# Optimization experiments

Measured on AMD Instinct MI355X. Metric: run time of the kernel, lower is better.

The kernel has to match this reference:

```python
import jax, jax.numpy as jnp
import numpy as np

B, S, F, D, H, L = 32, 512, 40, 512, 8, 4
T = S + 1
DK, DV = D // 2, D          # expand_k=0.5, expand_v=1.0 (fla GLA defaults)
HK, HV = DK // H, DV // H
GLR = 16                    # gate low-rank dim
GLN = 16.0                  # gate logit normalizer
MLP = 4 * D


def sin_pos(t, d, n=10000.0):
    pos = jnp.arange(t, dtype=jnp.float32)[:, None]
    den = jnp.power(n, 2.0 * jnp.arange(d // 2, dtype=jnp.float32) / d)
    e = jnp.zeros((t, d), jnp.float32)
    e = e.at[:, 0::2].set(jnp.sin(pos / den))
    e = e.at[:, 1::2].set(jnp.cos(pos / den))
    return e


def layernorm(x, w, b, eps=1e-5):
    m = x.mean(-1, keepdims=True)
    v = ((x - m) ** 2).mean(-1, keepdims=True)
    return (x - m) * jax.lax.rsqrt(v + eps) * w + b


def bin_norm(x, l1, b1, l2, b2, y1, y2):
    # x: (b, f, s). BiN: temporal z-norm with per-feature affine (X2) +
    # feature z-norm with per-time affine (X1); unbiased std, small std -> 1.
    st = jnp.sqrt(x.var(axis=2, ddof=1, keepdims=True))
    st = jnp.where(st < 1e-4, 1.0, st)
    Z2 = (x - x.mean(axis=2, keepdims=True)) / st
    X2 = l2[None, :, None] * Z2 + b2[None, :, None]
    sf = jnp.sqrt(x.var(axis=1, ddof=1, keepdims=True))
    sf = jnp.where(sf < 1e-4, 1.0, sf)
    Z1 = (x - x.mean(axis=1, keepdims=True)) / sf
    X1 = l1[None, None, :] * Z1 + b1[None, None, :]
    return y1 * X1 + y2 * X2


def gla_attn(x, qw, kw, vw, gw, gkw1, gkw2, gkb2, gnw, ow):
    # Gated linear attention, recurrent form: S_t = exp(gk_t) * S_{t-1} + k_t v_t^T
    b, t, _ = x.shape
    q = (x @ qw).reshape(b, t, H, HK) * (HK ** -0.5)
    k = (x @ kw).reshape(b, t, H, HK)
    v = (x @ vw).reshape(b, t, H, HV)
    g = (x @ gw).reshape(b, t, H, HV)
    gk = (jax.nn.log_sigmoid((x @ gkw1) @ gkw2 + gkb2) / GLN).reshape(b, t, H, HK)

    def step(Sc, inp):
        qt, kt, vt, gt = inp                       # (b,H,HK),(b,H,HK),(b,H,HV),(b,H,HK)
        Sc = Sc * jnp.exp(gt)[..., None] + kt[..., None] * vt[..., None, :]
        return Sc, jnp.einsum('bhk,bhkv->bhv', qt, Sc)

    init = jnp.zeros((b, H, HK, HV), x.dtype)
    to_t = lambda a: jnp.swapaxes(a, 0, 1)        # (t, b, H, dim)
    _, o = jax.lax.scan(step, init, (to_t(q), to_t(k), to_t(v), to_t(gk)))
    o = jnp.swapaxes(o, 0, 1)                     # (b, t, H, HV)
    o = o * jax.lax.rsqrt((o * o).mean(-1, keepdims=True) + 1e-5) * gnw  # head RMSNorm
    o = o * g * jax.nn.sigmoid(g)                 # swish output gate
    return o.reshape(b, t, DV) @ ow


def setup_inputs():
    key = jax.random.key(0)
    ks = iter(jax.random.split(key, 64))
    r = lambda shape, s=0.02: jax.random.normal(next(ks), shape, jnp.float32) * s
    return dict(
        x=jax.random.normal(next(ks), (B, S, F), jnp.float32),
        bin_l1=r((S,), 0.1), bin_b1=jnp.zeros((S,), jnp.float32),
        bin_l2=r((F,), 0.1), bin_b2=jnp.zeros((F,), jnp.float32),
        bin_y1=jnp.float32(0.5), bin_y2=jnp.float32(0.5),
        emb_w=r((F, D)), emb_b=jnp.zeros((D,), jnp.float32),
        cls_token=jnp.zeros((D,), jnp.float32),
        ln1_w=jnp.ones((L, D), jnp.float32), ln1_b=jnp.zeros((L, D), jnp.float32),
        q_w=r((L, D, DK)), k_w=r((L, D, DK)), v_w=r((L, D, DV)), g_w=r((L, D, DV)),
        gk_w1=r((L, D, GLR)), gk_w2=r((L, GLR, DK)), gk_b2=jnp.zeros((L, DK), jnp.float32),
        gnorm_w=jnp.ones((L, HV), jnp.float32),
        o_w=r((L, DV, D)),
        ln2_w=jnp.ones((L, D), jnp.float32), ln2_b=jnp.zeros((L, D), jnp.float32),
        mlp_w1=r((L, D, MLP)), mlp_b1=jnp.zeros((L, MLP), jnp.float32),
        mlp_w2=r((L, MLP, D)), mlp_b2=jnp.zeros((L, D), jnp.float32),
        head_w=r((D, 3)), head_b=jnp.zeros((3,), jnp.float32),
    )


def reference(x, bin_l1, bin_b1, bin_l2, bin_b2, bin_y1, bin_y2, emb_w, emb_b,
              cls_token, ln1_w, ln1_b, q_w, k_w, v_w, g_w, gk_w1, gk_w2, gk_b2,
              gnorm_w, o_w, ln2_w, ln2_b, mlp_w1, mlp_b1, mlp_w2, mlp_b2,
              head_w, head_b):
    h = bin_norm(jnp.swapaxes(x, 1, 2), bin_l1, bin_b1, bin_l2, bin_b2, bin_y1, bin_y2)
    h = jnp.swapaxes(h, 1, 2) @ emb_w + emb_b                    # (b, s, D)
    cls = jnp.broadcast_to(cls_token, (h.shape[0], 1, D))
    h = jnp.concatenate([h, cls], axis=1) + sin_pos(T, D)[None]  # (b, s+1, D)
    for i in range(L):
        a = gla_attn(layernorm(h, ln1_w[i], ln1_b[i]), q_w[i], k_w[i], v_w[i],
                     g_w[i], gk_w1[i], gk_w2[i], gk_b2[i], gnorm_w[i], o_w[i])
        h = h + a
        m = layernorm(h, ln2_w[i], ln2_b[i])
        m = jax.nn.gelu(m @ mlp_w1[i] + mlp_b1[i], approximate=False)
        h = h + m @ mlp_w2[i] + mlp_b2[i]
    return h[:, -1] @ head_w + head_b                            # (b, 3)
```

## Files before the change

### kernel.cpp

```cpp
#include <hip/hip_runtime.h>
#include <hip/hip_bf16.h>
#include <math.h>

#define Bsz   32
#define Ssz   512
#define Fsz   40
#define Dsz   512
#define Hh    8
#define Lnum  4
#define Tsz   513
#define DKsz  256
#define DVsz  512
#define HKsz  32
#define HVsz  64
#define Msz   (Bsz*Tsz)
#define Mpad  16512
#define MLPsz 2048
#define NCH   8
#define CSZ   65
#define QKVG  1536

typedef __attribute__((ext_vector_type(4))) float f32x4;
typedef __attribute__((ext_vector_type(8))) short bf16x8;

__device__ __forceinline__ float bf2f(short s) {
  unsigned int u = ((unsigned int)(unsigned short)s) << 16;
  return __builtin_bit_cast(float, u);
}
__device__ __forceinline__ short f2bf(float f) {
  __hip_bfloat16 b = __float2bfloat16(f);
  return __builtin_bit_cast(short, b);
}

__device__ __forceinline__ float wave_sum(float v) {
#pragma unroll
  for (int off = 32; off > 0; off >>= 1) v += __shfl_xor(v, off, 64);
  return v;
}

__global__ void pos_kernel(float* __restrict__ pos) {
  int idx = blockIdx.x * 256 + threadIdx.x;
  if (idx >= Tsz * Dsz) return;
  int t = idx / Dsz, d = idx % Dsz;
  float e = (float)(2 * (d >> 1)) / (float)Dsz;
  float den = powf(10000.f, e);
  float a = (float)t / den;
  pos[idx] = (d & 1) ? cosf(a) : sinf(a);
}

__global__ void tstat_kernel(const float* __restrict__ x,
                             float* __restrict__ mt, float* __restrict__ rst) {
  int bf = blockIdx.x;
  int b = bf / Fsz, f = bf % Fsz;
  int lane = threadIdx.x;
  const float* xp = x + (size_t)b * Ssz * Fsz + f;
  float s = 0.f, sq = 0.f;
  for (int i = lane; i < Ssz; i += 64) {
    float v = xp[(size_t)i * Fsz];
    s += v; sq += v * v;
  }
  s = wave_sum(s); sq = wave_sum(sq);
  if (lane == 0) {
    float m = s / (float)Ssz;
    float var = (sq - (float)Ssz * m * m) / (float)(Ssz - 1);
    float st = sqrtf(fmaxf(var, 0.f));
    if (st < 1e-4f) st = 1.f;
    mt[bf] = m;
    rst[bf] = 1.f / st;
  }
}

__global__ __launch_bounds__(64) void binorm_kernel(
    const float* __restrict__ x, const float* __restrict__ l1,
    const float* __restrict__ b1, const float* __restrict__ l2,
    const float* __restrict__ b2, const float* __restrict__ y1p,
    const float* __restrict__ y2p, const float* __restrict__ mt,
    const float* __restrict__ rst, float* __restrict__ xbT) {
  int row = blockIdx.x;
  int lane = threadIdx.x;
  int b = row / Tsz, t = row % Tsz;
  bool valid = (row < Msz) && (t < Ssz);
  if (!valid) {
    if (lane < Fsz) xbT[(size_t)lane * Mpad + row] = 0.f;
    return;
  }
  float xv = 0.f;
  const float* xp = x + ((size_t)b * Ssz + t) * Fsz;
  if (lane < Fsz) xv = xp[lane];
  float s  = wave_sum(lane < Fsz ? xv : 0.f);
  float sq = wave_sum(lane < Fsz ? xv * xv : 0.f);
  float m = s / (float)Fsz;
  float var = (sq - (float)Fsz * m * m) / (float)(Fsz - 1);
  float sf = sqrtf(fmaxf(var, 0.f));
  if (sf < 1e-4f) sf = 1.f;
  if (lane < Fsz) {
    float y1 = y1p[0], y2 = y2p[0];
    float z1 = (xv - m) / sf;
    float X1 = l1[t] * z1 + b1[t];
    int bf = b * Fsz + lane;
    float z2 = (xv - mt[bf]) * rst[bf];
    float X2 = l2[lane] * z2 + b2[lane];
    xbT[(size_t)lane * Mpad + row] = y1 * X1 + y2 * X2;
  }
}

__global__ __launch_bounds__(256, 4) void embgemm_kernel(
    const float* __restrict__ xbT, const float* __restrict__ emb_w,
    const float* __restrict__ emb_b, const float* __restrict__ cls,
    const float* __restrict__ pos, float* __restrict__ h) {
  __shared__ float as[Fsz][64];
  __shared__ float bs[Fsz][64];
  int tid = threadIdx.x, tx = tid & 15, ty = tid >> 4;
  int r0 = blockIdx.x * 64, c0 = blockIdx.y * 64;
  for (int idx = tid; idx < Fsz * 64; idx += 256) {
    int f = idx >> 6, r = idx & 63;
    as[f][r] = xbT[(size_t)f * Mpad + r0 + r];
    bs[f][r] = emb_w[f * Dsz + c0 + r];
  }
  __syncthreads();
  float acc[4][4] = {};
#pragma unroll 5
  for (int f = 0; f < Fsz; ++f) {
    float4 a = *(const float4*)&as[f][ty * 4];
    float4 bv = *(const float4*)&bs[f][tx * 4];
    float av[4] = {a.x, a.y, a.z, a.w};
    float bw[4] = {bv.x, bv.y, bv.z, bv.w};
#pragma unroll
    for (int i = 0; i < 4; ++i)
#pragma unroll
      for (int j = 0; j < 4; ++j) acc[i][j] += av[i] * bw[j];
  }
#pragma unroll
  for (int i = 0; i < 4; ++i) {
    int gm = r0 + ty * 4 + i;
    int t = gm % Tsz;
    const float* pp = pos + (size_t)t * Dsz;
    bool iscls = (t == Ssz);
    int gn = c0 + tx * 4;
#pragma unroll
    for (int j = 0; j < 4; ++j) {
      float v = iscls ? (cls[gn + j] + pp[gn + j])
                      : (acc[i][j] + emb_b[gn + j] + pp[gn + j]);
      h[(size_t)gm * Dsz + gn + j] = v;
    }
  }
}

__global__ __launch_bounds__(64) void ln_kernel(
    const float* __restrict__ in, const float* __restrict__ w,
    const float* __restrict__ b, short* __restrict__ out) {
  int row = blockIdx.x, lane = threadIdx.x;
  const float* p = in + (size_t)row * Dsz;
  float4 v0 = *(const float4*)(p + lane * 8);
  float4 v1 = *(const float4*)(p + lane * 8 + 4);
  float s  = v0.x + v0.y + v0.z + v0.w + v1.x + v1.y + v1.z + v1.w;
  float sq = v0.x*v0.x + v0.y*v0.y + v0.z*v0.z + v0.w*v0.w
           + v1.x*v1.x + v1.y*v1.y + v1.z*v1.z + v1.w*v1.w;
  s = wave_sum(s); sq = wave_sum(sq);
  float m = s * (1.f / Dsz);
  float var = sq * (1.f / Dsz) - m * m;
  float r = rsqrtf(var + 1e-5f);
  float4 w0 = *(const float4*)(w + lane * 8);
  float4 w1 = *(const float4*)(w + lane * 8 + 4);
  float4 b0 = *(const float4*)(b + lane * 8);
  float4 b1v = *(const float4*)(b + lane * 8 + 4);
  bf16x8 pk;
  pk[0] = f2bf((v0.x - m) * r * w0.x + b0.x);
  pk[1] = f2bf((v0.y - m) * r * w0.y + b0.y);
  pk[2] = f2bf((v0.z - m) * r * w0.z + b0.z);
  pk[3] = f2bf((v0.w - m) * r * w0.w + b0.w);
  pk[4] = f2bf((v1.x - m) * r * w1.x + b1v.x);
  pk[5] = f2bf((v1.y - m) * r * w1.y + b1v.y);
  pk[6] = f2bf((v1.z - m) * r * w1.z + b1v.z);
  pk[7] = f2bf((v1.w - m) * r * w1.w + b1v.w);
  *(bf16x8*)(out + (size_t)row * Dsz + lane * 8) = pk;
}

__global__ __launch_bounds__(256) void wt_kernel(const float* __restrict__ W,
    short* __restrict__ Wt, int K, int N) {
  __shared__ float t[32][33];
  int k0 = blockIdx.x * 32, n0 = blockIdx.y * 32;
  int tx = threadIdx.x & 31, ty = threadIdx.x >> 5;
#pragma unroll
  for (int r = 0; r < 32; r += 8)
    t[ty + r][tx] = W[(size_t)(k0 + ty + r) * N + n0 + tx];
  __syncthreads();
#pragma unroll
  for (int r = 0; r < 32; r += 8)
    Wt[(size_t)(n0 + ty + r) * K + k0 + tx] = f2bf(t[tx][ty + r]);
}

__global__ __launch_bounds__(256) void wt4_kernel(const float* __restrict__ qw,
    const float* __restrict__ kw, const float* __restrict__ vw,
    const float* __restrict__ gw, short* __restrict__ Wt) {
  __shared__ float t[32][33];
  int k0 = blockIdx.x * 32, n0g = blockIdx.y * 32;
  const float* W; int n0, ld;
  if (n0g < 256)       { W = qw; n0 = n0g;        ld = DKsz; }
  else if (n0g < 512)  { W = kw; n0 = n0g - 256;  ld = DKsz; }
  else if (n0g < 1024) { W = vw; n0 = n0g - 512;  ld = DVsz; }
  else                 { W = gw; n0 = n0g - 1024; ld = DVsz; }
  int tx = threadIdx.x & 31, ty = threadIdx.x >> 5;
#pragma unroll
  for (int r = 0; r < 32; r += 8)
    t[ty + r][tx] = W[(size_t)(k0 + ty + r) * ld + n0 + tx];
  __syncthreads();
#pragma unroll
  for (int r = 0; r < 32; r += 8)
    Wt[(size_t)(n0g + ty + r) * Dsz + k0 + tx] = f2bf(t[tx][ty + r]);
}

template<int ACT, int OBF>
__global__ __launch_bounds__(256) void mgemm_kernel(
    const short* __restrict__ A, const short* __restrict__ Bt,
    void* __restrict__ Cv, const float* __restrict__ bias,
    const float* __restrict__ resid, int N, int K) {
  __shared__ short As[128 * 64];
  __shared__ short Bs[128 * 64];
  int tid = threadIdx.x;
  int lane = tid & 63, wid = tid >> 6;
  int wr = wid >> 1, wc = wid & 1;
  int m0 = blockIdx.x * 128, n0 = blockIdx.y * 128;
  f32x4 acc[4][4];
#pragma unroll
  for (int i = 0; i < 4; ++i)
#pragma unroll
    for (int j = 0; j < 4; ++j) acc[i][j] = (f32x4){0.f, 0.f, 0.f, 0.f};

  int kq = lane >> 4;
  int rsel = lane & 15;

  for (int kt = 0; kt < K; kt += 64) {
#pragma unroll
    for (int i = 0; i < 4; ++i) {
      int li = i * 256 + tid;
      int row = li >> 3;
      int gsrc = (li & 7) ^ (row & 7);
      const short* ga = A + (size_t)(m0 + row) * K + kt + gsrc * 8;
      const short* gb = Bt + (size_t)(n0 + row) * K + kt + gsrc * 8;
      int base = (i * 256 + wid * 64) * 8;
      __builtin_amdgcn_global_load_lds(
          (const __attribute__((address_space(1))) unsigned int*)ga,
          (__attribute__((address_space(3))) unsigned int*)&As[base], 16, 0, 0);
      __builtin_amdgcn_global_load_lds(
          (const __attribute__((address_space(1))) unsigned int*)gb,
          (__attribute__((address_space(3))) unsigned int*)&Bs[base], 16, 0, 0);
    }
    __syncthreads();
#pragma unroll
    for (int s = 0; s < 2; ++s) {
      bf16x8 af[4], bfr[4];
#pragma unroll
      for (int i = 0; i < 4; ++i) {
        int row = wr * 64 + i * 16 + rsel;
        int slot = (s * 4 + kq) ^ (row & 7);
        af[i] = *(const bf16x8*)&As[row * 64 + slot * 8];
        int col = wc * 64 + i * 16 + rsel;
        int slotB = (s * 4 + kq) ^ (col & 7);
        bfr[i] = *(const bf16x8*)&Bs[col * 64 + slotB * 8];
      }
#pragma unroll
      for (int i = 0; i < 4; ++i)
#pragma unroll
        for (int j = 0; j < 4; ++j)
          acc[i][j] = __builtin_amdgcn_mfma_f32_16x16x32_bf16(af[i], bfr[j], acc[i][j], 0, 0, 0);
    }
    __syncthreads();
  }

#pragma unroll
  for (int i = 0; i < 4; ++i) {
    int rbase = m0 + wr * 64 + i * 16 + (lane >> 4) * 4;
#pragma unroll
    for (int j = 0; j < 4; ++j) {
      int gn = n0 + wc * 64 + j * 16 + (lane & 15);
      float bv = bias ? bias[gn] : 0.f;
#pragma unroll
      for (int r = 0; r < 4; ++r) {
        int gm = rbase + r;
        float v = acc[i][j][r] + bv;
        if (ACT == 1) v = 0.5f * v * (1.f + erff(v * 0.70710678118654752f));
        if (resid) v += resid[(size_t)gm * N + gn];
        if (OBF) ((short*)Cv)[(size_t)gm * N + gn] = f2bf(v);
        else     ((float*)Cv)[(size_t)gm * N + gn] = v;
      }
    }
  }
}

__global__ __launch_bounds__(64) void gk1_kernel(const short* __restrict__ xn,
    const float* __restrict__ w1, float* __restrict__ gk1) {
  int m = blockIdx.x, lane = threadIdx.x;
  __shared__ float xr[512];
  bf16x8 v = *(const bf16x8*)(xn + (size_t)m * Dsz + lane * 8);
#pragma unroll
  for (int e = 0; e < 8; ++e) xr[lane * 8 + e] = bf2f(v[e]);
  __syncthreads();
  int c = lane & 15, q = lane >> 4;
  float acc = 0.f;
#pragma unroll 8
  for (int i = 0; i < 128; ++i) {
    int k = q * 128 + i;
    acc += xr[k] * w1[k * 16 + c];
  }
  acc += __shfl_xor(acc, 16, 64);
  acc += __shfl_xor(acc, 32, 64);
  if (lane < 16) gk1[(size_t)m * 16 + c] = acc;
}

__global__ __launch_bounds__(256) void gk2_kernel(
    const float* __restrict__ gk1, const float* __restrict__ w2,
    const float* __restrict__ b2, float* __restrict__ gke) {
  int m = blockIdx.x, n = threadIdx.x;
  __shared__ float row[16];
  if (n < 16) row[n] = gk1[(size_t)m * 16 + n];
  __syncthreads();
  float acc = b2[n];
#pragma unroll
  for (int kk = 0; kk < 16; ++kk) acc += row[kk] * w2[kk * 256 + n];
  float z = acc;
  float ls = (z >= 0.f) ? -log1pf(expf(-z)) : z - log1pf(expf(z));
  gke[(size_t)m * 256 + n] = expf(ls * 0.0625f);
}

__global__ __launch_bounds__(64) void scanA_kernel(
    const float* __restrict__ qkvg, const float* __restrict__ gke,
    float* __restrict__ Ac, float* __restrict__ Bc) {
  int gid = blockIdx.x;
  int bh = gid >> 3, c = gid & 7;
  int b = bh >> 3, hh = bh & 7;
  int lane = threadIdx.x;
  int t0 = c * CSZ, t1 = min(t0 + CSZ, Tsz);
  const size_t rb = (size_t)b * Tsz;
  float S[32];
#pragma unroll
  for (int i = 0; i < 32; ++i) S[i] = 0.f;
  float ac = 1.f;
  for (int t = t0; t < t1; ++t) {
    const float* base = qkvg + (rb + t) * QKVG;
    const float* krow = base + 256 + hh * HKsz;
    const float* grow = gke + (rb + t) * DKsz + hh * HKsz;
    float vv = base[512 + hh * HVsz + lane];
    float gl = grow[lane & 31];
    float4 kr[8], gr[8];
#pragma unroll
    for (int j = 0; j < 8; ++j) {
      kr[j] = *(const float4*)(krow + j * 4);
      gr[j] = *(const float4*)(grow + j * 4);
    }
#pragma unroll
    for (int j = 0; j < 8; ++j) {
      S[4*j+0] = S[4*j+0] * gr[j].x + kr[j].x * vv;
      S[4*j+1] = S[4*j+1] * gr[j].y + kr[j].y * vv;
      S[4*j+2] = S[4*j+2] * gr[j].z + kr[j].z * vv;
      S[4*j+3] = S[4*j+3] * gr[j].w + kr[j].w * vv;
    }
    ac *= gl;
  }
  float* bp = Bc + ((size_t)gid * 64 + lane) * 32;
#pragma unroll
  for (int j = 0; j < 8; ++j)
    *(float4*)(bp + j * 4) = make_float4(S[4*j+0], S[4*j+1], S[4*j+2], S[4*j+3]);
  if (lane < 32) Ac[(size_t)gid * 32 + lane] = ac;
}

__global__ __launch_bounds__(64) void scanB_kernel(
    const float* __restrict__ Ac, float* __restrict__ Bc) {
  int bh = blockIdx.x;
  int lane = threadIdx.x;
  float cur[32];
#pragma unroll
  for (int i = 0; i < 32; ++i) cur[i] = 0.f;
  __shared__ float sA[32];
  for (int c = 0; c < NCH; ++c) {
    size_t gid = (size_t)bh * NCH + c;
    float* bp = Bc + (gid * 64 + lane) * 32;
    __syncthreads();
    if (lane < 32) sA[lane] = Ac[gid * 32 + lane];
    __syncthreads();
    float4 tb[8];
#pragma unroll
    for (int j = 0; j < 8; ++j) tb[j] = *(const float4*)(bp + j * 4);
#pragma unroll
    for (int j = 0; j < 8; ++j)
      *(float4*)(bp + j * 4) = make_float4(cur[4*j+0], cur[4*j+1], cur[4*j+2], cur[4*j+3]);
#pragma unroll
    for (int j = 0; j < 8; ++j) {
      cur[4*j+0] = sA[4*j+0] * cur[4*j+0] + tb[j].x;
      cur[4*j+1] = sA[4*j+1] * cur[4*j+1] + tb[j].y;
      cur[4*j+2] = sA[4*j+2] * cur[4*j+2] + tb[j].z;
      cur[4*j+3] = sA[4*j+3] * cur[4*j+3] + tb[j].w;
    }
  }
}

__global__ __launch_bounds__(64) void scanC_kernel(
    const float* __restrict__ qkvg, const float* __restrict__ gke,
    const float* __restrict__ gnw, const float* __restrict__ Bc,
    short* __restrict__ att) {
  int gid = blockIdx.x;
  int bh = gid >> 3, c = gid & 7;
  int b = bh >> 3, hh = bh & 7;
  int lane = threadIdx.x;
  int t0 = c * CSZ, t1 = min(t0 + CSZ, Tsz);
  const size_t rb = (size_t)b * Tsz;
  float S[32];
  const float* sp = Bc + ((size_t)gid * 64 + lane) * 32;
#pragma unroll
  for (int j = 0; j < 8; ++j) {
    float4 sv4 = *(const float4*)(sp + j * 4);
    S[4*j+0] = sv4.x; S[4*j+1] = sv4.y; S[4*j+2] = sv4.z; S[4*j+3] = sv4.w;
  }
  float gn = gnw[lane];
  for (int t = t0; t < t1; ++t) {
    const float* base = qkvg + (rb + t) * QKVG;
    const float* qrow = base + hh * HKsz;
    const float* krow = base + 256 + hh * HKsz;
    const float* grow = gke + (rb + t) * DKsz + hh * HKsz;
    float vv = base[512 + hh * HVsz + lane];
    float gv = base[1024 + hh * HVsz + lane];
    float4 kr[8], gr[8], qr[8];
#pragma unroll
    for (int j = 0; j < 8; ++j) {
      qr[j] = *(const float4*)(qrow + j * 4);
      kr[j] = *(const float4*)(krow + j * 4);
      gr[j] = *(const float4*)(grow + j * 4);
    }
    float o = 0.f;
#pragma unroll
    for (int j = 0; j < 8; ++j) {
      S[4*j+0] = S[4*j+0] * gr[j].x + kr[j].x * vv;  o += qr[j].x * S[4*j+0];
      S[4*j+1] = S[4*j+1] * gr[j].y + kr[j].y * vv;  o += qr[j].y * S[4*j+1];
      S[4*j+2] = S[4*j+2] * gr[j].z + kr[j].z * vv;  o += qr[j].z * S[4*j+2];
      S[4*j+3] = S[4*j+3] * gr[j].w + kr[j].w * vv;  o += qr[j].w * S[4*j+3];
    }
    o *= 0.17677669529663689f;
    float ss = wave_sum(o * o);
    float r = rsqrtf(ss * (1.f / 64.f) + 1e-5f);
    float sig = 1.f / (1.f + expf(-gv));
    att[((rb + t) * DVsz) + hh * HVsz + lane] = f2bf(o * r * gn * gv * sig);
  }
}

__global__ __launch_bounds__(64) void head_kernel(
    const float* __restrict__ h, const float* __restrict__ hw,
    const float* __restrict__ hb, float* __restrict__ out) {
  int b = blockIdx.x, lane = threadIdx.x;
  const float* p = h + ((size_t)b * Tsz + Ssz) * Dsz;
  float p0 = 0.f, p1 = 0.f, p2 = 0.f;
#pragma unroll
  for (int j = 0; j < 8; ++j) {
    int d = lane + j * 64;
    float hv = p[d];
    p0 += hv * hw[d * 3 + 0];
    p1 += hv * hw[d * 3 + 1];
    p2 += hv * hw[d * 3 + 2];
  }
  p0 = wave_sum(p0); p1 = wave_sum(p1); p2 = wave_sum(p2);
  if (lane == 0) {
    out[b * 3 + 0] = p0 + hb[0];
    out[b * 3 + 1] = p1 + hb[1];
    out[b * 3 + 2] = p2 + hb[2];
  }
}

extern "C" void kernel_launch(void* const* d_in, const int* in_sizes, int n_in,
                              void* d_out, int out_size, void* d_ws, size_t ws_size,
                              hipStream_t stream) {
  const float* x       = (const float*)d_in[0];
  const float* bin_l1  = (const float*)d_in[1];
  const float* bin_b1  = (const float*)d_in[2];
  const float* bin_l2  = (const float*)d_in[3];
  const float* bin_b2  = (const float*)d_in[4];
  const float* bin_y1  = (const float*)d_in[5];
  const float* bin_y2  = (const float*)d_in[6];
  const float* emb_w   = (const float*)d_in[7];
  const float* emb_b   = (const float*)d_in[8];
  const float* cls     = (const float*)d_in[9];
  const float* ln1_w   = (const float*)d_in[10];
  const float* ln1_b   = (const float*)d_in[11];
  const float* q_w     = (const float*)d_in[12];
  const float* k_w     = (const float*)d_in[13];
  const float* v_w     = (const float*)d_in[14];
  const float* g_w     = (const float*)d_in[15];
  const float* gk_w1   = (const float*)d_in[16];
  const float* gk_w2   = (const float*)d_in[17];
  const float* gk_b2   = (const float*)d_in[18];
  const float* gnorm_w = (const float*)d_in[19];
  const float* o_w     = (const float*)d_in[20];
  const float* ln2_w   = (const float*)d_in[21];
  const float* ln2_b   = (const float*)d_in[22];
  const float* mlp_w1  = (const float*)d_in[23];
  const float* mlp_b1  = (const float*)d_in[24];
  const float* mlp_w2  = (const float*)d_in[25];
  const float* mlp_b2  = (const float*)d_in[26];
  const float* head_w  = (const float*)d_in[27];
  const float* head_b  = (const float*)d_in[28];
  float* out = (float*)d_out;

  char* wptr = (char*)d_ws;
  auto alloc = [&](size_t bytes) { char* p = wptr; wptr += (bytes + 255) & ~(size_t)255; return p; };
  float* pos  = (float*)alloc((size_t)Tsz * Dsz * 4);
  float* h    = (float*)alloc((size_t)Mpad * Dsz * 4);
  short* xn   = (short*)alloc((size_t)Mpad * Dsz * 2);
  float* qkvg = (float*)alloc((size_t)Mpad * QKVG * 4);
  float* gkeb = (float*)alloc((size_t)Mpad * DKsz * 4);
  float* gk1b = (float*)alloc((size_t)Mpad * 16 * 4);
  float* mt   = (float*)alloc((size_t)Bsz * Fsz * 4);
  float* rst  = (float*)alloc((size_t)Bsz * Fsz * 4);
  float* Ac   = (float*)alloc((size_t)Bsz * Hh * NCH * 32 * 4);
  float* Bc   = (float*)alloc((size_t)Bsz * Hh * NCH * 64 * 32 * 4);
  short* wtr  = (short*)alloc((size_t)3145728 * 2);
  float* xbT  = qkvg;
  short* mid  = (short*)qkvg;
  short* att  = xn;

  short* qkvgT = wtr;
  short* owT   = qkvgT + 786432;
  short* m1T   = owT + 262144;
  short* m2T   = m1T + 1048576;

  hipLaunchKernelGGL(pos_kernel, dim3((Tsz * Dsz + 255) / 256), dim3(256), 0, stream, pos);
  hipLaunchKernelGGL(tstat_kernel, dim3(Bsz * Fsz), dim3(64), 0, stream, x, mt, rst);
  hipLaunchKernelGGL(binorm_kernel, dim3(Mpad), dim3(64), 0, stream,
                     x, bin_l1, bin_b1, bin_l2, bin_b2, bin_y1, bin_y2, mt, rst, xbT);
  hipLaunchKernelGGL(embgemm_kernel, dim3(258, 8), dim3(256), 0, stream,
                     xbT, emb_w, emb_b, cls, pos, h);

  dim3 blk256(256);
  for (int l = 0; l < Lnum; ++l) {
    hipLaunchKernelGGL(wt4_kernel, dim3(16, 48), blk256, 0, stream,
                       q_w + (size_t)l*Dsz*DKsz, k_w + (size_t)l*Dsz*DKsz,
                       v_w + (size_t)l*Dsz*DVsz, g_w + (size_t)l*Dsz*DVsz, qkvgT);
    hipLaunchKernelGGL(wt_kernel, dim3(16, 16), blk256, 0, stream, o_w   + (size_t)l*DVsz*Dsz,  owT, DVsz, Dsz);
    hipLaunchKernelGGL(wt_kernel, dim3(16, 64), blk256, 0, stream, mlp_w1+ (size_t)l*Dsz*MLPsz, m1T, Dsz, MLPsz);
    hipLaunchKernelGGL(wt_kernel, dim3(64, 16), blk256, 0, stream, mlp_w2+ (size_t)l*MLPsz*Dsz, m2T, MLPsz, Dsz);

    const float* lw1 = ln1_w + l * Dsz;  const float* lb1 = ln1_b + l * Dsz;
    const float* g1w = gk_w1 + (size_t)l * Dsz * 16;
    const float* g2w = gk_w2 + (size_t)l * 16 * DKsz;
    const float* g2b = gk_b2 + (size_t)l * DKsz;
    const float* gnw = gnorm_w + l * HVsz;
    const float* lw2 = ln2_w + l * Dsz;  const float* lb2 = ln2_b + l * Dsz;
    const float* m1b = mlp_b1 + (size_t)l * MLPsz;
    const float* m2b = mlp_b2 + (size_t)l * Dsz;

    hipLaunchKernelGGL(ln_kernel, dim3(Msz), dim3(64), 0, stream, h, lw1, lb1, xn);

    hipLaunchKernelGGL((mgemm_kernel<0,0>), dim3(129, 12), blk256, 0, stream,
                       xn, qkvgT, (void*)qkvg, (const float*)nullptr, (const float*)nullptr, QKVG, Dsz);
    hipLaunchKernelGGL(gk1_kernel, dim3(Msz), dim3(64), 0, stream, xn, g1w, gk1b);
    hipLaunchKernelGGL(gk2_kernel, dim3(Msz), blk256, 0, stream, gk1b, g2w, g2b, gkeb);

    hipLaunchKernelGGL(scanA_kernel, dim3(Bsz * Hh * NCH), dim3(64), 0, stream,
                       qkvg, gkeb, Ac, Bc);
    hipLaunchKernelGGL(scanB_kernel, dim3(Bsz * Hh), dim3(64), 0, stream, Ac, Bc);
    hipLaunchKernelGGL(scanC_kernel, dim3(Bsz * Hh * NCH), dim3(64), 0, stream,
                       qkvg, gkeb, gnw, Bc, att);

    hipLaunchKernelGGL((mgemm_kernel<0,0>), dim3(129, 4), blk256, 0, stream,
                       att, owT, (void*)h, (const float*)nullptr, h, Dsz, DVsz);

    hipLaunchKernelGGL(ln_kernel, dim3(Msz), dim3(64), 0, stream, h, lw2, lb2, xn);
    hipLaunchKernelGGL((mgemm_kernel<1,1>), dim3(129, 16), blk256, 0, stream,
                       xn, m1T, (void*)mid, m1b, (const float*)nullptr, MLPsz, Dsz);
    hipLaunchKernelGGL((mgemm_kernel<0,0>), dim3(129, 4), blk256, 0, stream,
                       mid, m2T, (void*)h, m2b, h, Dsz, MLPsz);
  }

  hipLaunchKernelGGL(head_kernel, dim3(Bsz), dim3(64), 0, stream, h, head_w, head_b, out);
}
```

Before: 1.806 ms.

## Scatter QKVG to head-major layout, stage scan chunks in LDS, double chunk count

The QKVG GEMM epilogue now scatters q/k and v into per-(batch,head) contiguous fp32 buffers and the output gate into fp16. gk2 writes gates in the same head-major layout. The scan kernels use 16 chunks of 33 steps instead of 8 of 65, and prefetch each chunk into LDS with global_load_lds rather than doing strided per-step global loads. This is meant to make scan memory access contiguous and raise parallelism. The cost is scattered GEMM stores, more LDS use, and reduced precision for the gate.

```diff
diff --git a/kernel.cpp b/kernel.cpp
--- a/kernel.cpp
+++ b/kernel.cpp
@@ -1,5 +1,6 @@
 #include <hip/hip_runtime.h>
 #include <hip/hip_bf16.h>
+#include <hip/hip_fp16.h>
 #include <math.h>
 
 #define Bsz   32
@@ -16,9 +17,10 @@
 #define Msz   (Bsz*Tsz)
 #define Mpad  16512
 #define MLPsz 2048
-#define NCH   8
-#define CSZ   65
+#define NCH   16
+#define CSZ   33
 #define QKVG  1536
+#define VOFF  8404992
 
 typedef __attribute__((ext_vector_type(4))) float f32x4;
 typedef __attribute__((ext_vector_type(8))) short bf16x8;
@@ -210,7 +212,7 @@
     Wt[(size_t)(n0g + ty + r) * Dsz + k0 + tx] = f2bf(t[tx][ty + r]);
 }
 
-template<int ACT, int OBF>
+template<int ACT, int OBF, int SCAT>
 __global__ __launch_bounds__(256) void mgemm_kernel(
     const short* __restrict__ A, const short* __restrict__ Bt,
     void* __restrict__ Cv, const float* __restrict__ bias,
@@ -274,15 +276,32 @@
 #pragma unroll
     for (int j = 0; j < 4; ++j) {
       int gn = n0 + wc * 64 + j * 16 + (lane & 15);
-      float bv = bias ? bias[gn] : 0.f;
+      float bv = (SCAT == 0 && bias) ? bias[gn] : 0.f;
 #pragma unroll
       for (int r = 0; r < 4; ++r) {
         int gm = rbase + r;
         float v = acc[i][j][r] + bv;
-        if (ACT == 1) v = 0.5f * v * (1.f + erff(v * 0.70710678118654752f));
-        if (resid) v += resid[(size_t)gm * N + gn];
-        if (OBF) ((short*)Cv)[(size_t)gm * N + gn] = f2bf(v);
-        else     ((float*)Cv)[(size_t)gm * N + gn] = v;
+        if (SCAT == 0) {
+          if (ACT == 1) v = 0.5f * v * (1.f + erff(v * 0.70710678118654752f));
+          if (resid) v += resid[(size_t)gm * N + gn];
+          if (OBF) ((short*)Cv)[(size_t)gm * N + gn] = f2bf(v);
+          else     ((float*)Cv)[(size_t)gm * N + gn] = v;
+        } else {
+          if (gm < Msz) {
+            int bq = gm / Tsz, tq = gm - bq * Tsz;
+            if (gn < 512) {
+              int hq = (gn >> 5) & 7;
+              int off = (gn & 31) | ((gn & 256) >> 3);
+              ((float*)Cv)[(((size_t)bq * 8 + hq) * Tsz + tq) * 64 + off] = v;
+            } else if (gn < 1024) {
+              int hq = (gn >> 6) & 7;
+              ((float*)Cv)[(size_t)VOFF + (((size_t)bq * 8 + hq) * Tsz + tq) * 64 + (gn & 63)] = v;
+            } else {
+              int hq = (gn >> 6) & 7;
+              ((__half*)const_cast<float*>(resid))[(((size_t)bq * 8 + hq) * Tsz + tq) * 64 + (gn & 63)] = __float2half(v);
+            }
+          }
+        }
       }
     }
   }
@@ -310,7 +329,7 @@
 
 __global__ __launch_bounds__(256) void gk2_kernel(
     const float* __restrict__ gk1, const float* __restrict__ w2,
-    const float* __restrict__ b2, float* __restrict__ gke) {
+    const float* __restrict__ b2, float* __restrict__ gkeP) {
   int m = blockIdx.x, n = threadIdx.x;
   __shared__ float row[16];
   if (n < 16) row[n] = gk1[(size_t)m * 16 + n];
@@ -320,42 +339,66 @@
   for (int kk = 0; kk < 16; ++kk) acc += row[kk] * w2[kk * 256 + n];
   float z = acc;
   float ls = (z >= 0.f) ? -log1pf(expf(-z)) : z - log1pf(expf(z));
-  gke[(size_t)m * 256 + n] = expf(ls * 0.0625f);
+  int b = m / Tsz, t = m - b * Tsz;
+  int h = n >> 5;
+  gkeP[(((size_t)b * 8 + h) * Tsz + t) * 32 + (n & 31)] = expf(ls * 0.0625f);
 }
 
 __global__ __launch_bounds__(64) void scanA_kernel(
-    const float* __restrict__ qkvg, const float* __restrict__ gke,
+    const float* __restrict__ qkP, const float* __restrict__ gkeP,
     float* __restrict__ Ac, float* __restrict__ Bc) {
   int gid = blockIdx.x;
-  int bh = gid >> 3, c = gid & 7;
-  int b = bh >> 3, hh = bh & 7;
+  int bh = gid >> 4, c = gid & 15;
   int lane = threadIdx.x;
-  int t0 = c * CSZ, t1 = min(t0 + CSZ, Tsz);
-  const size_t rb = (size_t)b * Tsz;
+  int t0 = c * CSZ;
+  int nst = min(CSZ, Tsz - t0);
+  __shared__ __align__(16) float s_k[CSZ * 32];
+  __shared__ __align__(16) float s_g[CSZ * 32];
+  __shared__ __align__(16) float s_v[CSZ * 64];
+  const size_t rowbase = (size_t)bh * Tsz + t0;
+  const float* qksrc = qkP + rowbase * 64;
+  const float* vsrc  = qkP + (size_t)VOFF + rowbase * 64;
+  const float* gsrc  = gkeP + rowbase * 32;
+  int nkg = nst * 8;
+#pragma unroll
+  for (int i = 0; i < 5; ++i) {
+    int gi = i * 64 + lane;
+    if (gi < nkg) {
+      int st = gi >> 3, g4 = (gi & 7) * 4;
+      __builtin_amdgcn_global_load_lds(
+        (const __attribute__((address_space(1))) unsigned int*)(qksrc + (size_t)st * 64 + 32 + g4),
+        (__attribute__((address_space(3))) unsigned int*)s_k + i * 256, 16, 0, 0);
+      __builtin_amdgcn_global_load_lds(
+        (const __attribute__((address_space(1))) unsigned int*)(gsrc + (size_t)gi * 4),
+        (__attribute__((address_space(3))) unsigned int*)s_g + i * 256, 16, 0, 0);
+    }
+  }
+  int nv = nst * 16;
+#pragma unroll
+  for (int i = 0; i < 9; ++i) {
+    int gi = i * 64 + lane;
+    if (gi < nv)
+      __builtin_amdgcn_global_load_lds(
+        (const __attribute__((address_space(1))) unsigned int*)(vsrc + (size_t)gi * 4),
+        (__attribute__((address_space(3))) unsigned int*)s_v + i * 256, 16, 0, 0);
+  }
   float S[32];
 #pragma unroll
   for (int i = 0; i < 32; ++i) S[i] = 0.f;
   float ac = 1.f;
-  for (int t = t0; t < t1; ++t) {
-    const float* base = qkvg + (rb + t) * QKVG;
-    const float* krow = base + 256 + hh * HKsz;
-    const float* grow = gke + (rb + t) * DKsz + hh * HKsz;
-    float vv = base[512 + hh * HVsz + lane];
-    float gl = grow[lane & 31];
-    float4 kr[8], gr[8];
+  __syncthreads();
+  for (int ts = 0; ts < nst; ++ts) {
+    float vv = s_v[ts * 64 + lane];
 #pragma unroll
     for (int j = 0; j < 8; ++j) {
-      kr[j] = *(const float4*)(krow + j * 4);
-      gr[j] = *(const float4*)(grow + j * 4);
-    }
-#pragma unroll
-    for (int j = 0; j < 8; ++j) {
-      S[4*j+0] = S[4*j+0] * gr[j].x + kr[j].x * vv;
-      S[4*j+1] = S[4*j+1] * gr[j].y + kr[j].y * vv;
-      S[4*j+2] = S[4*j+2] * gr[j].z + kr[j].z * vv;
-      S[4*j+3] = S[4*j+3] * gr[j].w + kr[j].w * vv;
-    }
-    ac *= gl;
+      float4 kk = *(const float4*)&s_k[ts * 32 + j * 4];
+      float4 gg = *(const float4*)&s_g[ts * 32 + j * 4];
+      S[4*j+0] = S[4*j+0] * gg.x + kk.x * vv;
+      S[4*j+1] = S[4*j+1] * gg.y + kk.y * vv;
+      S[4*j+2] = S[4*j+2] * gg.z + kk.z * vv;
+      S[4*j+3] = S[4*j+3] * gg.w + kk.w * vv;
+    }
+    ac *= s_g[ts * 32 + (lane & 31)];
   }
   float* bp = Bc + ((size_t)gid * 64 + lane) * 32;
 #pragma unroll
@@ -395,15 +438,50 @@
 }
 
 __global__ __launch_bounds__(64) void scanC_kernel(
-    const float* __restrict__ qkvg, const float* __restrict__ gke,
-    const float* __restrict__ gnw, const float* __restrict__ Bc,
-    short* __restrict__ att) {
+    const float* __restrict__ qkP, const __half* __restrict__ gP,
+    const float* __restrict__ gkeP, const float* __restrict__ gnw,
+    const float* __restrict__ Bc, short* __restrict__ att) {
   int gid = blockIdx.x;
-  int bh = gid >> 3, c = gid & 7;
+  int bh = gid >> 4, c = gid & 15;
   int b = bh >> 3, hh = bh & 7;
   int lane = threadIdx.x;
-  int t0 = c * CSZ, t1 = min(t0 + CSZ, Tsz);
-  const size_t rb = (size_t)b * Tsz;
+  int t0 = c * CSZ;
+  int nst = min(CSZ, Tsz - t0);
+  __shared__ __align__(16) float s_qk[CSZ * 64];
+  __shared__ __align__(16) float s_g[CSZ * 32];
+  __shared__ __align__(16) float s_v[CSZ * 64];
+  __shared__ __align__(16) __half s_gt[CSZ * 64];
+  const size_t rowbase = (size_t)bh * Tsz + t0;
+  const float* qksrc = qkP + rowbase * 64;
+  const float* vsrc  = qkP + (size_t)VOFF + rowbase * 64;
+  const float* gsrc  = gkeP + rowbase * 32;
+  const __half* gtsrc = gP + rowbase * 64;
+  int n16 = nst * 16;
+#pragma unroll
+  for (int i = 0; i < 9; ++i) {
+    int gi = i * 64 + lane;
+    if (gi < n16) {
+      __builtin_amdgcn_global_load_lds(
+        (const __attribute__((address_space(1))) unsigned int*)(qksrc + (size_t)gi * 4),
+        (__attribute__((address_space(3))) unsigned int*)s_qk + i * 256, 16, 0, 0);
+      __builtin_amdgcn_global_load_lds(
+        (const __attribute__((address_space(1))) unsigned int*)(vsrc + (size_t)gi * 4),
+        (__attribute__((address_space(3))) unsigned int*)s_v + i * 256, 16, 0, 0);
+    }
+  }
+  int n8 = nst * 8;
+#pragma unroll
+  for (int i = 0; i < 5; ++i) {
+    int gi = i * 64 + lane;
+    if (gi < n8) {
+      __builtin_amdgcn_global_load_lds(
+        (const __attribute__((address_space(1))) unsigned int*)(gsrc + (size_t)gi * 4),
+        (__attribute__((address_space(3))) unsigned int*)s_g + i * 256, 16, 0, 0);
+      __builtin_amdgcn_global_load_lds(
+        (const __attribute__((address_space(1))) unsigned int*)((const unsigned int*)gtsrc + (size_t)gi * 4),
+        (__attribute__((address_space(3))) unsigned int*)s_gt + i * 256, 16, 0, 0);
+    }
+  }
   float S[32];
   const float* sp = Bc + ((size_t)gid * 64 + lane) * 32;
 #pragma unroll
@@ -412,33 +490,26 @@
     S[4*j+0] = sv4.x; S[4*j+1] = sv4.y; S[4*j+2] = sv4.z; S[4*j+3] = sv4.w;
   }
   float gn = gnw[lane];
-  for (int t = t0; t < t1; ++t) {
-    const float* base = qkvg + (rb + t) * QKVG;
-    const float* qrow = base + hh * HKsz;
-    const float* krow = base + 256 + hh * HKsz;
-    const float* grow = gke + (rb + t) * DKsz + hh * HKsz;
-    float vv = base[512 + hh * HVsz + lane];
-    float gv = base[1024 + hh * HVsz + lane];
-    float4 kr[8], gr[8], qr[8];
+  __syncthreads();
+  for (int ts = 0; ts < nst; ++ts) {
+    float vv = s_v[ts * 64 + lane];
+    float gv = __half2float(s_gt[ts * 64 + lane]);
+    float o = 0.f;
 #pragma unroll
     for (int j = 0; j < 8; ++j) {
-      qr[j] = *(const float4*)(qrow + j * 4);
-      kr[j] = *(const float4*)(krow + j * 4);
-      gr[j] = *(const float4*)(grow + j * 4);
-    }
-    float o = 0.f;
-#pragma unroll
-    for (int j = 0; j < 8; ++j) {
-      S[4*j+0] = S[4*j+0] * gr[j].x + kr[j].x * vv;  o += qr[j].x * S[4*j+0];
-      S[4*j+1] = S[4*j+1] * gr[j].y + kr[j].y * vv;  o += qr[j].y * S[4*j+1];
-      S[4*j+2] = S[4*j+2] * gr[j].z + kr[j].z * vv;  o += qr[j].z * S[4*j+2];
-      S[4*j+3] = S[4*j+3] * gr[j].w + kr[j].w * vv;  o += qr[j].w * S[4*j+3];
+      float4 qq = *(const float4*)&s_qk[ts * 64 + j * 4];
+      float4 kk = *(const float4*)&s_qk[ts * 64 + 32 + j * 4];
+      float4 gg = *(const float4*)&s_g[ts * 32 + j * 4];
+      S[4*j+0] = S[4*j+0] * gg.x + kk.x * vv;  o += qq.x * S[4*j+0];
+      S[4*j+1] = S[4*j+1] * gg.y + kk.y * vv;  o += qq.y * S[4*j+1];
+      S[4*j+2] = S[4*j+2] * gg.z + kk.z * vv;  o += qq.z * S[4*j+2];
+      S[4*j+3] = S[4*j+3] * gg.w + kk.w * vv;  o += qq.w * S[4*j+3];
     }
     o *= 0.17677669529663689f;
     float ss = wave_sum(o * o);
     float r = rsqrtf(ss * (1.f / 64.f) + 1e-5f);
     float sig = 1.f / (1.f + expf(-gv));
-    att[((rb + t) * DVsz) + hh * HVsz + lane] = f2bf(o * r * gn * gv * sig);
+    att[((size_t)b * Tsz + t0 + ts) * DVsz + hh * HVsz + lane] = f2bf(o * r * gn * gv * sig);
   }
 }
 
@@ -503,22 +574,23 @@
   float* pos  = (float*)alloc((size_t)Tsz * Dsz * 4);
   float* h    = (float*)alloc((size_t)Mpad * Dsz * 4);
   short* xn   = (short*)alloc((size_t)Mpad * Dsz * 2);
-  float* qkvg = (float*)alloc((size_t)Mpad * QKVG * 4);
-  float* gkeb = (float*)alloc((size_t)Mpad * DKsz * 4);
+  float* qkP  = (float*)alloc((size_t)Mpad * MLPsz * 2);
+  float* gkeP = (float*)alloc((size_t)256 * Tsz * 32 * 4);
+  __half* gP  = (__half*)alloc((size_t)256 * Tsz * 64 * 2);
   float* gk1b = (float*)alloc((size_t)Mpad * 16 * 4);
   float* mt   = (float*)alloc((size_t)Bsz * Fsz * 4);
   float* rst  = (float*)alloc((size_t)Bsz * Fsz * 4);
   float* Ac   = (float*)alloc((size_t)Bsz * Hh * NCH * 32 * 4);
   float* Bc   = (float*)alloc((size_t)Bsz * Hh * NCH * 64 * 32 * 4);
   short* wtr  = (short*)alloc((size_t)3145728 * 2);
-  float* xbT  = qkvg;
-  short* mid  = (short*)qkvg;
+  float* xbT  = qkP;
+  short* mid  = (short*)qkP;
   short* att  = xn;
 
-  short* qkvgT = wtr;
-  short* owT   = qkvgT + 786432;
-  short* m1T   = owT + 262144;
-  short* m2T   = m1T + 1048576;
+  short* qkvT = wtr;
+  short* owT  = qkvT + 786432;
+  short* m1T  = owT + 262144;
+  short* m2T  = m1T + 1048576;
 
   hipLaunchKernelGGL(pos_kernel, dim3((Tsz * Dsz + 255) / 256), dim3(256), 0, stream, pos);
   hipLaunchKernelGGL(tstat_kernel, dim3(Bsz * Fsz), dim3(64), 0, stream, x, mt, rst);
@@ -531,7 +603,7 @@
   for (int l = 0; l < Lnum; ++l) {
     hipLaunchKernelGGL(wt4_kernel, dim3(16, 48), blk256, 0, stream,
                        q_w + (size_t)l*Dsz*DKsz, k_w + (size_t)l*Dsz*DKsz,
-                       v_w + (size_t)l*Dsz*DVsz, g_w + (size_t)l*Dsz*DVsz, qkvgT);
+                       v_w + (size_t)l*Dsz*DVsz, g_w + (size_t)l*Dsz*DVsz, qkvT);
     hipLaunchKernelGGL(wt_kernel, dim3(16, 16), blk256, 0, stream, o_w   + (size_t)l*DVsz*Dsz,  owT, DVsz, Dsz);
     hipLaunchKernelGGL(wt_kernel, dim3(16, 64), blk256, 0, stream, mlp_w1+ (size_t)l*Dsz*MLPsz, m1T, Dsz, MLPsz);
     hipLaunchKernelGGL(wt_kernel, dim3(64, 16), blk256, 0, stream, mlp_w2+ (size_t)l*MLPsz*Dsz, m2T, MLPsz, Dsz);
@@ -547,24 +619,24 @@
 
     hipLaunchKernelGGL(ln_kernel, dim3(Msz), dim3(64), 0, stream, h, lw1, lb1, xn);
 
-    hipLaunchKernelGGL((mgemm_kernel<0,0>), dim3(129, 12), blk256, 0, stream,
-                       xn, qkvgT, (void*)qkvg, (const float*)nullptr, (const float*)nullptr, QKVG, Dsz);
+    hipLaunchKernelGGL((mgemm_kernel<0,0,1>), dim3(129, 12), blk256, 0, stream,
+                       xn, qkvT, (void*)qkP, (const float*)nullptr, (const float*)gP, QKVG, Dsz);
     hipLaunchKernelGGL(gk1_kernel, dim3(Msz), dim3(64), 0, stream, xn, g1w, gk1b);
-    hipLaunchKernelGGL(gk2_kernel, dim3(Msz), blk256, 0, stream, gk1b, g2w, g2b, gkeb);
+    hipLaunchKernelGGL(gk2_kernel, dim3(Msz), blk256, 0, stream, gk1b, g2w, g2b, gkeP);
 
     hipLaunchKernelGGL(scanA_kernel, dim3(Bsz * Hh * NCH), dim3(64), 0, stream,
-                       qkvg, gkeb, Ac, Bc);
+                       qkP, gkeP, Ac, Bc);
     hipLaunchKernelGGL(scanB_kernel, dim3(Bsz * Hh), dim3(64), 0, stream, Ac, Bc);
     hipLaunchKernelGGL(scanC_kernel, dim3(Bsz * Hh * NCH), dim3(64), 0, stream,
-                       qkvg, gkeb, gnw, Bc, att);
-
-    hipLaunchKernelGGL((mgemm_kernel<0,0>), dim3(129, 4), blk256, 0, stream,
+                       qkP, gP, gkeP, gnw, Bc, att);
+
+    hipLaunchKernelGGL((mgemm_kernel<0,0,0>), dim3(129, 4), blk256, 0, stream,
                        att, owT, (void*)h, (const float*)nullptr, h, Dsz, DVsz);
 
     hipLaunchKernelGGL(ln_kernel, dim3(Msz), dim3(64), 0, stream, h, lw2, lb2, xn);
-    hipLaunchKernelGGL((mgemm_kernel<1,1>), dim3(129, 16), blk256, 0, stream,
+    hipLaunchKernelGGL((mgemm_kernel<1,1,0>), dim3(129, 16), blk256, 0, stream,
                        xn, m1T, (void*)mid, m1b, (const float*)nullptr, MLPsz, Dsz);
-    hipLaunchKernelGGL((mgemm_kernel<0,0>), dim3(129, 4), blk256, 0, stream,
+    hipLaunchKernelGGL((mgemm_kernel<0,0,0>), dim3(129, 4), blk256, 0, stream,
                        mid, m2T, (void*)h, m2b, h, Dsz, MLPsz);
   }
 
```

New measurement: 1.805 ms. No clear change (-0.1%).
